# Kernel tuning notes

Hardware: AMD Instinct MI355X
Metric: run time of the kernel (lower is better)

Reference implementation:

```python
import math
import jax, jax.numpy as jnp
import numpy as np

D_MODEL = 1024
N_HEADS = 16
HEAD_DIM = D_MODEL // N_HEADS  # 64
QDIM = HEAD_DIM // 4           # 16
SPIKE_SLOPE = 5.0
B, S = 2, 2048


def _qweight(r, i, j, k):
    # Hamilton-product weight matrix, identical to QLinear.forward's torch.cat construction.
    return jnp.concatenate([
        jnp.concatenate([r, -i, -j, -k], 1),
        jnp.concatenate([i, r, -k, j], 1),
        jnp.concatenate([j, k, r, -i], 1),
        jnp.concatenate([k, -j, i, r], 1),
    ], 0)


def setup_inputs() -> dict:
    key = jax.random.key(0)
    ks = jax.random.split(key, 20)
    Qo = Qi = D_MODEL // 4  # 256
    p = lambda k, shape, s=0.02: (jax.random.normal(k, shape, dtype=jnp.float32) * s)
    inp = {
        'query': jax.random.normal(ks[0], (B, S, D_MODEL), dtype=jnp.float32),
        'key_in': jax.random.normal(ks[1], (B, S, D_MODEL), dtype=jnp.float32),
        'value': jax.random.normal(ks[2], (B, S, D_MODEL), dtype=jnp.float32),
        'mask': jnp.ones((B, S), dtype=jnp.int32),
        'density_feat': jax.random.normal(ks[3], (B, S, 3), dtype=jnp.float32),
        # q_proj QLinear params
        'wq_r': p(ks[4], (Qo, Qi)), 'wq_i': p(ks[5], (Qo, Qi)),
        'wq_j': p(ks[6], (Qo, Qi)), 'wq_k': p(ks[7], (Qo, Qi)),
        'bq': jnp.zeros((D_MODEL,), jnp.float32),
        # k_proj QLinear params
        'wk_r': p(ks[8], (Qo, Qi)), 'wk_i': p(ks[9], (Qo, Qi)),
        'wk_j': p(ks[10], (Qo, Qi)), 'wk_k': p(ks[11], (Qo, Qi)),
        'bk': jnp.zeros((D_MODEL,), jnp.float32),
        # v_proj / out_proj dense params
        'wv': p(ks[12], (D_MODEL, D_MODEL)), 'bv': jnp.zeros((D_MODEL,), jnp.float32),
        'wo': p(ks[13], (D_MODEL, D_MODEL)), 'bo': jnp.zeros((D_MODEL,), jnp.float32),
        # learned spike threshold (init -1.0 as in torch)
        'threshold': jnp.asarray(-1.0, dtype=jnp.float32),
        # density_mod MLP (use nonzero values so the gate shift is exercised)
        'dm1_w': p(ks[14], (16, 3), 0.5), 'dm1_b': p(ks[15], (16,), 0.1),
        'dm2_w': p(ks[16], (1, 16), 0.5), 'dm2_b': p(ks[17], (1,), 0.1),
    }
    return inp


def reference(query, key_in, value, mask, density_feat,
              wq_r, wq_i, wq_j, wq_k, bq,
              wk_r, wk_i, wk_j, wk_k, bk,
              wv, bv, wo, bo, threshold,
              dm1_w, dm1_b, dm2_w, dm2_b):
    H, hd, Qd = N_HEADS, HEAD_DIM, QDIM
    Bq, Sq, D = query.shape

    Wq = _qweight(wq_r, wq_i, wq_j, wq_k)
    Wk = _qweight(wk_r, wk_i, wk_j, wk_k)
    q = query @ Wq.T + bq
    k = key_in @ Wk.T + bk
    v = value @ wv.T + bv

    # head-major split, matching torch.cat(x.split(hd, -1), dim=0)
    qh = q.reshape(Bq, Sq, H, hd).transpose(2, 0, 1, 3)  # (H,B,S,hd)
    kh = k.reshape(Bq, Sq, H, hd).transpose(2, 0, 1, 3)
    vh = v.reshape(Bq, Sq, H, hd).transpose(2, 0, 1, 3)

    # sum of 4 quaternion-component dot products == full dot product over hd
    scores = jnp.einsum('hbmd,hbnd->hbmn', qh, kh) / math.sqrt(Qd)
    scores = jnp.clip(scores, -6.0, 6.0)

    base_threshold = jax.nn.softplus(threshold)
    h1 = jax.nn.gelu(density_feat @ dm1_w.T + dm1_b, approximate=False)
    d_shift = (h1 @ dm2_w.T + dm2_b)[..., 0]  # (B,N)
    thr = base_threshold + d_shift[None, :, None, :] * 0.1  # (1,B,1,N)

    spike_gate = jax.nn.sigmoid(SPIKE_SLOPE * (scores - thr))
    mod = scores * (1.0 + spike_gate * 2.0)

    m2 = (mask[:, :, None] * mask[:, None, :])[None]  # (1,B,N,N)
    mod = jnp.where(m2 == 0, -10000.0, mod)

    weights = jax.nn.softmax(jnp.clip(mod, -30.0, 30.0), axis=-1)
    # dropout: eval mode (identity)
    out_h = jnp.einsum('hbmn,hbnd->hbmd', weights, vh)
    out = out_h.transpose(1, 2, 0, 3).reshape(Bq, Sq, D)
    return out @ wo.T + bo
```

## Files before the change

kernel.cpp:

```cpp
#include <hip/hip_runtime.h>
#include <stdint.h>
#include <math.h>

#define BB 2
#define SS 2048
#define DM 1024
#define NH 16
#define HD 64
#define MTOT (BB*SS)

typedef __bf16 bf16x8 __attribute__((ext_vector_type(8)));
typedef float  f32x4  __attribute__((ext_vector_type(4)));
typedef uint32_t u32x4 __attribute__((ext_vector_type(4)));

__device__ __forceinline__ unsigned short f2bf(float f) {
  uint32_t u = __builtin_bit_cast(uint32_t, f);
  u += 0x7fffu + ((u >> 16) & 1u);
  return (unsigned short)(u >> 16);
}

__device__ __forceinline__ bf16x8 ldsv8(const unsigned short* p) {
  return __builtin_bit_cast(bf16x8, *(const u32x4*)p);
}

#define MFMA16(a,b,c) __builtin_amdgcn_mfma_f32_16x16x32_bf16((a),(b),(c),0,0,0)

#define C_NEG5L2E  (-7.213475204444817f)
#define C_L2E      (1.4426950408889634f)
#define C_18L2E    (25.968510736001341f)

__global__ __launch_bounds__(256) void prep_w(
    const float* __restrict__ wqr, const float* __restrict__ wqi,
    const float* __restrict__ wqj, const float* __restrict__ wqk,
    const float* __restrict__ wkr, const float* __restrict__ wki,
    const float* __restrict__ wkj, const float* __restrict__ wkk,
    const float* __restrict__ wv,  const float* __restrict__ wo,
    unsigned short* __restrict__ Wq, unsigned short* __restrict__ Wk,
    unsigned short* __restrict__ Wv, unsigned short* __restrict__ Wo)
{
  const int idx = blockIdx.x * 256 + threadIdx.x;
  const int o = idx >> 10, i = idx & 1023;
  const int br = o >> 8, bc = i >> 8;
  const int ro = o & 255, ci = i & 255;
  const int comp[4][4] = {{0,1,2,3},{1,0,3,2},{2,3,0,1},{3,2,1,0}};
  const float sgn[4][4] = {{1.f,-1.f,-1.f,-1.f},{1.f,1.f,-1.f,1.f},{1.f,1.f,1.f,-1.f},{1.f,-1.f,1.f,1.f}};
  const float* pq[4] = {wqr, wqi, wqj, wqk};
  const float* pk[4] = {wkr, wki, wkj, wkk};
  const int c_ = comp[br][bc];
  const float s_ = sgn[br][bc];
  const int pidx = ro * 256 + ci;
  Wq[idx] = f2bf(s_ * pq[c_][pidx]);
  Wk[idx] = f2bf(s_ * pk[c_][pidx]);
  Wv[idx] = f2bf(wv[idx]);
  Wo[idx] = f2bf(wo[idx]);
}

__global__ __launch_bounds__(256) void prep_thr(
    const float* __restrict__ density, const float* __restrict__ dm1w,
    const float* __restrict__ dm1b, const float* __restrict__ dm2w,
    const float* __restrict__ dm2b, const float* __restrict__ thr_s,
    const int* __restrict__ mask, float2* __restrict__ out)
{
  const int i = blockIdx.x * 256 + threadIdx.x;
  if (i >= BB * SS) return;
  const float x0 = density[i*3+0], x1 = density[i*3+1], x2 = density[i*3+2];
  const float base = log1pf(expf(thr_s[0]));
  float acc = dm2b[0];
  #pragma unroll
  for (int j = 0; j < 16; ++j) {
    const float hj = dm1w[j*3+0]*x0 + dm1w[j*3+1]*x1 + dm1w[j*3+2]*x2 + dm1b[j];
    const float ge = 0.5f * hj * (1.0f + erff(hj * 0.70710678118654752f));
    acc += dm2w[j] * ge;
  }
  const float thr = base + 0.1f * acc;
  out[i] = make_float2(thr * (-C_NEG5L2E),
                       mask[i] ? 1e30f : -30.0f);
}

template<int AMODE, int OMODE>
__global__ __launch_bounds__(256) void gemm_bt(const void* __restrict__ Aptr,
                                               const unsigned short* __restrict__ W,
                                               const float* __restrict__ bias,
                                               void* __restrict__ Cptr, float scale)
{
  __shared__ __align__(16) unsigned short lA[128*64];
  __shared__ __align__(16) unsigned short lB[128*64];
  const int tid = threadIdx.x;
  const int wid = tid >> 6, lane = tid & 63;
  const int l15 = lane & 15, l4 = lane >> 4;
  const int bm = blockIdx.x >> 3, bn = blockIdx.x & 7;
  const int row0 = bm * 128, col0 = bn * 128;
  const int wm = (wid >> 1) * 64, wn = (wid & 1) * 64;

  f32x4 acc[4][4];
  #pragma unroll
  for (int i = 0; i < 4; ++i)
    #pragma unroll
    for (int j = 0; j < 4; ++j) acc[i][j] = (f32x4){0.f,0.f,0.f,0.f};

  for (int kt = 0; kt < 16; ++kt) {
    const int k0 = kt * 64;
    #pragma unroll
    for (int it = 0; it < 4; ++it) {
      const int c = tid + it * 256;
      const int r = c >> 3, j = c & 7;
      const int didx = r * 64 + ((j * 8) ^ ((r & 7) << 3));
      if (AMODE == 0) {
        const float* src = (const float*)Aptr + (row0 + r) * 1024 + k0 + j * 8;
        const float4 f0 = *(const float4*)src;
        const float4 f1 = *(const float4*)(src + 4);
        union { unsigned short us[8]; u32x4 v; } tmp;
        tmp.us[0]=f2bf(f0.x); tmp.us[1]=f2bf(f0.y); tmp.us[2]=f2bf(f0.z); tmp.us[3]=f2bf(f0.w);
        tmp.us[4]=f2bf(f1.x); tmp.us[5]=f2bf(f1.y); tmp.us[6]=f2bf(f1.z); tmp.us[7]=f2bf(f1.w);
        *(u32x4*)&lA[didx] = tmp.v;
      } else {
        const unsigned short* src = (const unsigned short*)Aptr + (row0 + r) * 1024 + k0 + j * 8;
        *(u32x4*)&lA[didx] = *(const u32x4*)src;
      }
      const unsigned short* bsrc = W + (col0 + r) * 1024 + k0 + j * 8;
      *(u32x4*)&lB[didx] = *(const u32x4*)bsrc;
    }
    __syncthreads();
    #pragma unroll
    for (int kk = 0; kk < 2; ++kk) {
      const int kl = kk * 32 + l4 * 8;
      bf16x8 af[4], bfb[4];
      #pragma unroll
      for (int mi = 0; mi < 4; ++mi) {
        const int r = wm + mi * 16 + l15;
        af[mi] = ldsv8(&lA[r * 64 + (kl ^ ((r & 7) << 3))]);
      }
      #pragma unroll
      for (int nj = 0; nj < 4; ++nj) {
        const int r = wn + nj * 16 + l15;
        bfb[nj] = ldsv8(&lB[r * 64 + (kl ^ ((r & 7) << 3))]);
      }
      __builtin_amdgcn_s_setprio(1);
      #pragma unroll
      for (int mi = 0; mi < 4; ++mi)
        #pragma unroll
        for (int nj = 0; nj < 4; ++nj)
          acc[mi][nj] = MFMA16(af[mi], bfb[nj], acc[mi][nj]);
      __builtin_amdgcn_s_setprio(0);
    }
    __syncthreads();
  }
  #pragma unroll
  for (int nj = 0; nj < 4; ++nj) {
    const int c = col0 + wn + nj * 16 + l15;
    const float bv_ = bias[c];
    #pragma unroll
    for (int mi = 0; mi < 4; ++mi) {
      const int rb = row0 + wm + mi * 16 + l4 * 4;
      #pragma unroll
      for (int e = 0; e < 4; ++e) {
        const float val = (acc[mi][nj][e] + bv_) * scale;
        const int r = rb + e;
        if (OMODE == 0) {
          ((unsigned short*)Cptr)[r * 1024 + c] = f2bf(val);
        } else if (OMODE == 2) {
          ((float*)Cptr)[r * 1024 + c] = val;
        } else {
          const int h = c >> 6, d = c & 63, b = r >> 11, s = r & 2047;
          ((unsigned short*)Cptr)[((h * BB + b) * HD + d) * SS + s] = f2bf(val);
        }
      }
    }
  }
}

__global__ __launch_bounds__(256) void attn_kernel(
    const unsigned short* __restrict__ qg, const unsigned short* __restrict__ kg,
    const unsigned short* __restrict__ vT, const float2* __restrict__ klim,
    const int* __restrict__ mask, unsigned short* __restrict__ outg)
{
  __shared__ __align__(16) unsigned short lK[2][64*64];
  __shared__ __align__(16) unsigned short lV[2][64*64];
  __shared__ __align__(16) unsigned short lP[4][16*64];
  const int tid = threadIdx.x;
  const int wid = tid >> 6, lane = tid & 63;
  const int l15 = lane & 15, l4 = lane >> 4;
  const int qb = blockIdx.x & 31, hb = blockIdx.x >> 5;
  const int h = hb >> 1, b = hb & 1;
  const int qr0 = qb * 64 + wid * 16;

  const int c0r = tid >> 3, c0j = (tid & 7) * 8;
  const int c1r = c0r + 32;
  const int dK0 = c0r * 64 + (c0j ^ ((c0r & 7) << 3));
  const int dK1 = c1r * 64 + (c0j ^ ((c1r & 7) << 3));
  const unsigned short* kbase = kg + (b * SS) * DM + h * HD;
  const unsigned short* vbase = vT + ((h * BB + b) * HD) * SS;
  const float2* klimb = klim + b * SS;

  bf16x8 aq[2];
  {
    const unsigned short* qs = qg + (b * SS + qr0 + l15) * DM + h * HD + l4 * 8;
    aq[0] = __builtin_bit_cast(bf16x8, *(const u32x4*)qs);
    aq[1] = __builtin_bit_cast(bf16x8, *(const u32x4*)(qs + 32));
  }
  float limq[4];
  #pragma unroll
  for (int e = 0; e < 4; ++e)
    limq[e] = mask[b * SS + qr0 + l4 * 4 + e] ? 1e30f : -30.0f;

  float lrun[4] = {0.f, 0.f, 0.f, 0.f};
  f32x4 o[4];
  #pragma unroll
  for (int d = 0; d < 4; ++d) o[d] = (f32x4){0.f,0.f,0.f,0.f};

  unsigned short* lPw = lP[wid];

  u32x4 kr0 = *(const u32x4*)(kbase + c0r * DM + c0j);
  u32x4 kr1 = *(const u32x4*)(kbase + c1r * DM + c0j);
  u32x4 vr0 = *(const u32x4*)(vbase + c0r * SS + c0j);
  u32x4 vr1 = *(const u32x4*)(vbase + c1r * SS + c0j);
  *(u32x4*)&lK[0][dK0] = kr0;
  *(u32x4*)&lK[0][dK1] = kr1;
  *(u32x4*)&lV[0][dK0] = vr0;
  *(u32x4*)&lV[0][dK1] = vr1;
  __syncthreads();

  for (int kb = 0; kb < 32; ++kb) {
    const int cur = kb & 1;
    const unsigned short* lKc = lK[cur];
    const unsigned short* lVc = lV[cur];
    const int n0g = kb * 64;

    if (kb < 31) {
      const int n2 = n0g + 64;
      kr0 = *(const u32x4*)(kbase + (n2 + c0r) * DM + c0j);
      kr1 = *(const u32x4*)(kbase + (n2 + c1r) * DM + c0j);
      vr0 = *(const u32x4*)(vbase + c0r * SS + n2 + c0j);
      vr1 = *(const u32x4*)(vbase + c1r * SS + n2 + c0j);
    }

    float2 kl[4];
    #pragma unroll
    for (int cf = 0; cf < 4; ++cf) kl[cf] = klimb[n0g + cf * 16 + l15];

    f32x4 sv[4];
    __builtin_amdgcn_s_setprio(1);
    #pragma unroll
    for (int cf = 0; cf < 4; ++cf) {
      f32x4 a = (f32x4){0.f,0.f,0.f,0.f};
      #pragma unroll
      for (int kk = 0; kk < 2; ++kk) {
        const int n = cf * 16 + l15;
        bf16x8 bk_ = ldsv8(&lKc[n * 64 + ((kk * 32 + l4 * 8) ^ ((n & 7) << 3))]);
        a = MFMA16(aq[kk], bk_, a);
      }
      sv[cf] = a;
    }
    __builtin_amdgcn_s_setprio(0);

    float pvv[4][4];
    #pragma unroll
    for (int cf = 0; cf < 4; ++cf) {
      #pragma unroll
      for (int e = 0; e < 4; ++e) {
        float s = fminf(fmaxf(sv[cf][e], -6.f), 6.f);
        const float t = __builtin_amdgcn_exp2f(fmaf(s, C_NEG5L2E, kl[cf].x));
        const float g = __builtin_amdgcn_rcpf(1.f + t);
        float md = fmaf(s + s, g, s);
        md = fminf(md, fminf(kl[cf].y, limq[e]));
        const float p = __builtin_amdgcn_exp2f(fmaf(md, C_L2E, -C_18L2E));
        pvv[cf][e] = p;
        lrun[e] += p;
      }
    }

    #pragma unroll
    for (int cf = 0; cf < 4; ++cf)
      #pragma unroll
      for (int e = 0; e < 4; ++e) {
        const int rr = l4 * 4 + e, cc = cf * 16 + l15;
        lPw[rr * 64 + (cc ^ ((rr & 7) << 3))] = f2bf(pvv[cf][e]);
      }
    asm volatile("s_waitcnt lgkmcnt(0)" ::: "memory");
    __builtin_amdgcn_sched_barrier(0);

    bf16x8 pa[2];
    #pragma unroll
    for (int kk = 0; kk < 2; ++kk)
      pa[kk] = ldsv8(&lPw[l15 * 64 + ((kk * 32 + l4 * 8) ^ ((l15 & 7) << 3))]);

    __builtin_amdgcn_s_setprio(1);
    #pragma unroll
    for (int df = 0; df < 4; ++df) {
      #pragma unroll
      for (int kk = 0; kk < 2; ++kk) {
        const int d = df * 16 + l15;
        bf16x8 bv_ = ldsv8(&lVc[d * 64 + ((kk * 32 + l4 * 8) ^ ((d & 7) << 3))]);
        o[df] = MFMA16(pa[kk], bv_, o[df]);
      }
    }
    __builtin_amdgcn_s_setprio(0);

    if (kb < 31) {
      const int nxt = cur ^ 1;
      *(u32x4*)&lK[nxt][dK0] = kr0;
      *(u32x4*)&lK[nxt][dK1] = kr1;
      *(u32x4*)&lV[nxt][dK0] = vr0;
      *(u32x4*)&lV[nxt][dK1] = vr1;
    }
    __syncthreads();
  }

  #pragma unroll
  for (int e = 0; e < 4; ++e) {
    float ls = lrun[e];
    ls += __shfl_xor(ls, 1);
    ls += __shfl_xor(ls, 2);
    ls += __shfl_xor(ls, 4);
    ls += __shfl_xor(ls, 8);
    const float rl = __builtin_amdgcn_rcpf(ls);
    const int r = qr0 + l4 * 4 + e;
    #pragma unroll
    for (int df = 0; df < 4; ++df) {
      outg[(b * SS + r) * DM + h * HD + df * 16 + l15] = f2bf(o[df][e] * rl);
    }
  }
}

extern "C" void kernel_launch(void* const* d_in, const int* in_sizes, int n_in,
                              void* d_out, int out_size, void* d_ws, size_t ws_size,
                              hipStream_t stream)
{
  const float* query   = (const float*)d_in[0];
  const float* key_in  = (const float*)d_in[1];
  const float* value   = (const float*)d_in[2];
  const int*   mask    = (const int*)d_in[3];
  const float* density = (const float*)d_in[4];
  const float* wq_r = (const float*)d_in[5];
  const float* wq_i = (const float*)d_in[6];
  const float* wq_j = (const float*)d_in[7];
  const float* wq_k = (const float*)d_in[8];
  const float* bq   = (const float*)d_in[9];
  const float* wk_r = (const float*)d_in[10];
  const float* wk_i = (const float*)d_in[11];
  const float* wk_j = (const float*)d_in[12];
  const float* wk_k = (const float*)d_in[13];
  const float* bk   = (const float*)d_in[14];
  const float* wv   = (const float*)d_in[15];
  const float* bv   = (const float*)d_in[16];
  const float* wo   = (const float*)d_in[17];
  const float* bo   = (const float*)d_in[18];
  const float* thrs = (const float*)d_in[19];
  const float* dm1w = (const float*)d_in[20];
  const float* dm1b = (const float*)d_in[21];
  const float* dm2w = (const float*)d_in[22];
  const float* dm2b = (const float*)d_in[23];

  char* ws = (char*)d_ws;
  unsigned short* Wq  = (unsigned short*)(ws + ((size_t)0 << 20));
  unsigned short* Wk  = (unsigned short*)(ws + ((size_t)2 << 20));
  unsigned short* Wv  = (unsigned short*)(ws + ((size_t)4 << 20));
  unsigned short* Wo  = (unsigned short*)(ws + ((size_t)6 << 20));
  unsigned short* qbf = (unsigned short*)(ws + ((size_t)8 << 20));
  unsigned short* kbf = (unsigned short*)(ws + ((size_t)16 << 20));
  unsigned short* vT  = (unsigned short*)(ws + ((size_t)24 << 20));
  unsigned short* att = (unsigned short*)(ws + ((size_t)32 << 20));
  float2* klim        = (float2*)(ws + ((size_t)40 << 20));

  prep_w<<<4096, 256, 0, stream>>>(wq_r, wq_i, wq_j, wq_k,
                                   wk_r, wk_i, wk_j, wk_k,
                                   wv, wo, Wq, Wk, Wv, Wo);
  prep_thr<<<16, 256, 0, stream>>>(density, dm1w, dm1b, dm2w, dm2b, thrs, mask, klim);
  gemm_bt<0,0><<<256, 256, 0, stream>>>(query,  Wq, bq, qbf, 0.25f);
  gemm_bt<0,0><<<256, 256, 0, stream>>>(key_in, Wk, bk, kbf, 1.0f);
  gemm_bt<0,1><<<256, 256, 0, stream>>>(value,  Wv, bv, vT, 1.0f);
  attn_kernel<<<1024, 256, 0, stream>>>(qbf, kbf, vT, klim, mask, att);
  gemm_bt<1,2><<<256, 256, 0, stream>>>(att, Wo, bo, (float*)d_out, 1.0f);
}
```

Baseline: 216.9 us.

## Batch QKV GEMMs into one launch and load bf16 tiles via global_load_lds

Merges the three Q/K/V projection GEMMs into one launch using a blockIdx.y selector and a runtime output mode, which cuts launch overhead and gives the GPU 768 blocks to schedule at once. The bf16 operand tiles (weights, and the attention output in the final GEMM) are now copied straight from global memory into LDS with global_load_lds, keeping the XOR swizzle by permuting the source addresses. It also switches f32→bf16 conversion to the compiler's native cast and drops the s_setprio hints. The runtime omode branch in the epilogue and the loss of setprio could add some overhead.

```diff
diff --git a/kernel.cpp b/kernel.cpp
--- a/kernel.cpp
+++ b/kernel.cpp
@@ -14,13 +14,18 @@
 typedef uint32_t u32x4 __attribute__((ext_vector_type(4)));
 
 __device__ __forceinline__ unsigned short f2bf(float f) {
-  uint32_t u = __builtin_bit_cast(uint32_t, f);
-  u += 0x7fffu + ((u >> 16) & 1u);
-  return (unsigned short)(u >> 16);
+  __bf16 h = (__bf16)f;
+  return __builtin_bit_cast(unsigned short, h);
 }
 
 __device__ __forceinline__ bf16x8 ldsv8(const unsigned short* p) {
   return __builtin_bit_cast(bf16x8, *(const u32x4*)p);
+}
+
+__device__ __forceinline__ void gl16(const void* g, void* l) {
+  __builtin_amdgcn_global_load_lds(
+      (const __attribute__((address_space(1))) uint32_t*)g,
+      (__attribute__((address_space(3))) uint32_t*)l, 16, 0, 0);
 }
 
 #define MFMA16(a,b,c) __builtin_amdgcn_mfma_f32_16x16x32_bf16((a),(b),(c),0,0,0)
@@ -77,14 +82,22 @@
                        mask[i] ? 1e30f : -30.0f);
 }
 
-template<int AMODE, int OMODE>
-__global__ __launch_bounds__(256) void gemm_bt(const void* __restrict__ Aptr,
-                                               const unsigned short* __restrict__ W,
-                                               const float* __restrict__ bias,
-                                               void* __restrict__ Cptr, float scale)
+struct GemmArgs {
+  const void* A[3];
+  const unsigned short* W[3];
+  const float* bias[3];
+  void* out[3];
+  float scale[3];
+  int omode[3];
+};
+
+template<int AMODE>
+__global__ __launch_bounds__(256) void gemm_fused(GemmArgs args)
 {
   __shared__ __align__(16) unsigned short lA[128*64];
   __shared__ __align__(16) unsigned short lB[128*64];
+  const int z = blockIdx.y;
+  const unsigned short* W = args.W[z];
   const int tid = threadIdx.x;
   const int wid = tid >> 6, lane = tid & 63;
   const int l15 = lane & 15, l4 = lane >> 4;
@@ -92,6 +105,22 @@
   const int row0 = bm * 128, col0 = bn * 128;
   const int wm = (wid >> 1) * 64, wn = (wid & 1) * 64;
 
+  const unsigned short* gB[4];
+  unsigned short* dB[4];
+  const unsigned short* gA1[4];
+  unsigned short* dA1[4];
+  #pragma unroll
+  for (int i = 0; i < 4; ++i) {
+    const int c = (wid * 4 + i) * 64 + lane;
+    const int r = c >> 3, jx = c & 7, j = jx ^ (r & 7);
+    gB[i] = W + (col0 + r) * 1024 + j * 8;
+    dB[i] = &lB[(wid * 4 + i) * 512];
+    if (AMODE == 1) {
+      gA1[i] = (const unsigned short*)args.A[z] + (row0 + r) * 1024 + j * 8;
+      dA1[i] = &lA[(wid * 4 + i) * 512];
+    }
+  }
+
   f32x4 acc[4][4];
   #pragma unroll
   for (int i = 0; i < 4; ++i)
@@ -101,24 +130,24 @@
   for (int kt = 0; kt < 16; ++kt) {
     const int k0 = kt * 64;
     #pragma unroll
-    for (int it = 0; it < 4; ++it) {
-      const int c = tid + it * 256;
-      const int r = c >> 3, j = c & 7;
-      const int didx = r * 64 + ((j * 8) ^ ((r & 7) << 3));
-      if (AMODE == 0) {
-        const float* src = (const float*)Aptr + (row0 + r) * 1024 + k0 + j * 8;
+    for (int i = 0; i < 4; ++i) gl16(gB[i] + k0, dB[i]);
+    if (AMODE == 1) {
+      #pragma unroll
+      for (int i = 0; i < 4; ++i) gl16(gA1[i] + k0, dA1[i]);
+    } else {
+      #pragma unroll
+      for (int it = 0; it < 4; ++it) {
+        const int c = tid + it * 256;
+        const int r = c >> 3, j = c & 7;
+        const int didx = r * 64 + ((j * 8) ^ ((r & 7) << 3));
+        const float* src = (const float*)args.A[z] + (row0 + r) * 1024 + k0 + j * 8;
         const float4 f0 = *(const float4*)src;
         const float4 f1 = *(const float4*)(src + 4);
         union { unsigned short us[8]; u32x4 v; } tmp;
         tmp.us[0]=f2bf(f0.x); tmp.us[1]=f2bf(f0.y); tmp.us[2]=f2bf(f0.z); tmp.us[3]=f2bf(f0.w);
         tmp.us[4]=f2bf(f1.x); tmp.us[5]=f2bf(f1.y); tmp.us[6]=f2bf(f1.z); tmp.us[7]=f2bf(f1.w);
         *(u32x4*)&lA[didx] = tmp.v;
-      } else {
-        const unsigned short* src = (const unsigned short*)Aptr + (row0 + r) * 1024 + k0 + j * 8;
-        *(u32x4*)&lA[didx] = *(const u32x4*)src;
-      }
-      const unsigned short* bsrc = W + (col0 + r) * 1024 + k0 + j * 8;
-      *(u32x4*)&lB[didx] = *(const u32x4*)bsrc;
+      }
     }
     __syncthreads();
     #pragma unroll
@@ -135,30 +164,32 @@
         const int r = wn + nj * 16 + l15;
         bfb[nj] = ldsv8(&lB[r * 64 + (kl ^ ((r & 7) << 3))]);
       }
-      __builtin_amdgcn_s_setprio(1);
       #pragma unroll
       for (int mi = 0; mi < 4; ++mi)
         #pragma unroll
         for (int nj = 0; nj < 4; ++nj)
           acc[mi][nj] = MFMA16(af[mi], bfb[nj], acc[mi][nj]);
-      __builtin_amdgcn_s_setprio(0);
     }
     __syncthreads();
   }
+
+  const int om = args.omode[z];
+  const float sc = args.scale[z];
+  void* Cptr = args.out[z];
   #pragma unroll
   for (int nj = 0; nj < 4; ++nj) {
     const int c = col0 + wn + nj * 16 + l15;
-    const float bv_ = bias[c];
+    const float bv_ = args.bias[z][c];
     #pragma unroll
     for (int mi = 0; mi < 4; ++mi) {
       const int rb = row0 + wm + mi * 16 + l4 * 4;
       #pragma unroll
       for (int e = 0; e < 4; ++e) {
-        const float val = (acc[mi][nj][e] + bv_) * scale;
+        const float val = (acc[mi][nj][e] + bv_) * sc;
         const int r = rb + e;
-        if (OMODE == 0) {
+        if (om == 0) {
           ((unsigned short*)Cptr)[r * 1024 + c] = f2bf(val);
-        } else if (OMODE == 2) {
+        } else if (om == 2) {
           ((float*)Cptr)[r * 1024 + c] = val;
         } else {
           const int h = c >> 6, d = c & 63, b = r >> 11, s = r & 2047;
@@ -366,9 +397,18 @@
                                    wk_r, wk_i, wk_j, wk_k,
                                    wv, wo, Wq, Wk, Wv, Wo);
   prep_thr<<<16, 256, 0, stream>>>(density, dm1w, dm1b, dm2w, dm2b, thrs, mask, klim);
-  gemm_bt<0,0><<<256, 256, 0, stream>>>(query,  Wq, bq, qbf, 0.25f);
-  gemm_bt<0,0><<<256, 256, 0, stream>>>(key_in, Wk, bk, kbf, 1.0f);
-  gemm_bt<0,1><<<256, 256, 0, stream>>>(value,  Wv, bv, vT, 1.0f);
+
+  GemmArgs qkv;
+  qkv.A[0] = query;  qkv.W[0] = Wq; qkv.bias[0] = bq; qkv.out[0] = qbf; qkv.scale[0] = 0.25f; qkv.omode[0] = 0;
+  qkv.A[1] = key_in; qkv.W[1] = Wk; qkv.bias[1] = bk; qkv.out[1] = kbf; qkv.scale[1] = 1.0f;  qkv.omode[1] = 0;
+  qkv.A[2] = value;  qkv.W[2] = Wv; qkv.bias[2] = bv; qkv.out[2] = vT;  qkv.scale[2] = 1.0f;  qkv.omode[2] = 1;
+  gemm_fused<0><<<dim3(256, 3), 256, 0, stream>>>(qkv);
+
   attn_kernel<<<1024, 256, 0, stream>>>(qbf, kbf, vT, klim, mask, att);
-  gemm_bt<1,2><<<256, 256, 0, stream>>>(att, Wo, bo, (float*)d_out, 1.0f);
-}
+
+  GemmArgs og;
+  og.A[0] = att; og.W[0] = Wo; og.bias[0] = bo; og.out[0] = d_out; og.scale[0] = 1.0f; og.omode[0] = 2;
+  og.A[1] = att; og.W[1] = Wo; og.bias[1] = bo; og.out[1] = d_out; og.scale[1] = 1.0f; og.omode[1] = 2;
+  og.A[2] = att; og.W[2] = Wo; og.bias[2] = bo; og.out[2] = d_out; og.scale[2] = 1.0f; og.omode[2] = 2;
+  gemm_fused<1><<<dim3(256, 1), 256, 0, stream>>>(og);
+}
```

Measured after the change: 217.7 us. No clear change (+0.4%).
